# Optimization experiments

Hardware: AMD Instinct MI355X
Metric: run time of the kernel (lower is better)

The kernel has to match this reference:

```python
import jax, jax.numpy as jnp
import numpy as np

NUM_USERS = 100000
NUM_ITEMS = 10000
USER_DIM = 32
ITEM_DIM = 32
H1 = 128
H2 = 128
BATCH = 4096


def setup_inputs() -> dict:
    key = jax.random.key(0)
    ks = jax.random.split(key, 10)
    interactions = jax.random.randint(ks[0], (BATCH, 2), 0, NUM_ITEMS, dtype=jnp.int64)
    users_emb_w = jax.random.normal(ks[1], (NUM_USERS, USER_DIM), dtype=jnp.float32)
    items_emb_w = jax.random.normal(ks[2], (NUM_ITEMS, ITEM_DIM), dtype=jnp.float32)
    d_in = USER_DIM + ITEM_DIM
    w1 = jax.random.normal(ks[3], (H1, d_in), dtype=jnp.float32) / np.sqrt(d_in)
    b1 = jnp.zeros((H1,), dtype=jnp.float32)
    w2 = jax.random.normal(ks[4], (H2, H1), dtype=jnp.float32) / np.sqrt(H1)
    b2 = jnp.zeros((H2,), dtype=jnp.float32)
    head_in = NUM_ITEMS + H2
    w_head = jax.random.normal(ks[5], (NUM_ITEMS, head_in), dtype=jnp.float32) / np.sqrt(head_in)
    b_head = jnp.zeros((NUM_ITEMS,), dtype=jnp.float32)
    return {
        "interactions": interactions,
        "users_emb_w": users_emb_w,
        "items_emb_w": items_emb_w,
        "w1": w1, "b1": b1, "w2": w2, "b2": b2,
        "w_head": w_head, "b_head": b_head,
    }


def reference(interactions, users_emb_w, items_emb_w, w1, b1, w2, b2, w_head, b_head):
    users = interactions[:, 0]
    items = interactions[:, 1]
    # embedding lookups + concat -> [B, 64]
    all_embed = jnp.concatenate([users_emb_w[users], items_emb_w[items]], axis=1)
    # deep MLP (dropout p=0 -> identity)
    h = jax.nn.relu(all_embed @ w1.T + b1)
    h = jax.nn.relu(h @ w2.T + b2)
    # wide one-hot [B, num_items]
    cross = jax.nn.one_hot(items, NUM_ITEMS, dtype=h.dtype)
    head_in = jnp.concatenate([cross, h], axis=1)
    return jax.nn.sigmoid(head_in @ w_head.T + b_head)
```

## Files before the change

kernel.cpp:

```cpp
#include <hip/hip_runtime.h>


#define BATCH    4096
#define NITEMS   10000
#define HEADCOLS 10128
#define DENSEOFF 10000

typedef __attribute__((ext_vector_type(8))) short short8;
typedef __attribute__((ext_vector_type(4))) short short4v;
typedef __attribute__((ext_vector_type(4))) float floatx4;

__device__ inline unsigned short f2bf(float f) {
    unsigned u = __builtin_bit_cast(unsigned, f);
    unsigned r = (u + 0x7FFFu + ((u >> 16) & 1u)) >> 16;
    return (unsigned short)r;
}

__device__ inline float bf2f(unsigned short u) {
    unsigned x = ((unsigned)u) << 16;
    return __builtin_bit_cast(float, x);
}

__global__ __launch_bounds__(256) void k1_mlp(
    const int* __restrict__ inter,
    const float* __restrict__ U, const float* __restrict__ I,
    const float* __restrict__ w1, const float* __restrict__ b1,
    const float* __restrict__ w2, const float* __restrict__ b2,
    unsigned short* __restrict__ h2b)
{
    __shared__ float e_lds[8 * 64];
    __shared__ float h1_lds[8 * 128];
    const int t  = threadIdx.x;
    const int b0 = blockIdx.x * 8;

    for (int idx = t; idx < 8 * 64; idx += 256) {
        int b = idx >> 6, d = idx & 63;
        int u  = inter[2 * (b0 + b)];
        int it = inter[2 * (b0 + b) + 1];
        e_lds[idx] = (d < 32) ? U[(long)u * 32 + d] : I[(long)it * 32 + (d - 32)];
    }
    __syncthreads();

    const int i = t & 127;
    const int g = (t >> 7) * 4;

    {
        float acc[4];
        #pragma unroll
        for (int b = 0; b < 4; b++) acc[b] = b1[i];
        for (int d = 0; d < 64; d += 4) {
            float4 w = *(const float4*)&w1[i * 64 + d];
            #pragma unroll
            for (int b = 0; b < 4; b++) {
                float4 e = *(const float4*)&e_lds[(g + b) * 64 + d];
                acc[b] += w.x * e.x + w.y * e.y + w.z * e.z + w.w * e.w;
            }
        }
        #pragma unroll
        for (int b = 0; b < 4; b++) h1_lds[(g + b) * 128 + i] = fmaxf(acc[b], 0.f);
    }
    __syncthreads();

    {
        float acc[4];
        #pragma unroll
        for (int b = 0; b < 4; b++) acc[b] = b2[i];
        for (int k = 0; k < 128; k += 4) {
            float4 w = *(const float4*)&w2[i * 128 + k];
            #pragma unroll
            for (int b = 0; b < 4; b++) {
                float4 h = *(const float4*)&h1_lds[(g + b) * 128 + k];
                acc[b] += w.x * h.x + w.y * h.y + w.z * h.z + w.w * h.w;
            }
        }
        #pragma unroll
        for (int b = 0; b < 4; b++)
            h2b[(long)(b0 + g + b) * 128 + i] = f2bf(fmaxf(acc[b], 0.f));
    }
}

#define KG_ROWS 4
__global__ __launch_bounds__(256) void kg_gather(
    const int* __restrict__ inter,
    const float* __restrict__ w_head,
    unsigned short* __restrict__ wg,
    unsigned short* __restrict__ wd)
{
    __shared__ float row_lds[HEADCOLS];
    const int t  = threadIdx.x;
    const int j0 = blockIdx.x * KG_ROWS;

    int c0[8], c1[8];
    #pragma unroll
    for (int i = 0; i < 8; i++) {
        int p = t + 256 * i;
        c0[i] = inter[4 * p + 1];
        c1[i] = inter[4 * p + 3];
    }

    for (int r = 0; r < KG_ROWS; r++) {
        const float* row = w_head + (long)(j0 + r) * HEADCOLS;
        for (int idx = t; idx < HEADCOLS / 4; idx += 256) {
            floatx4 v = __builtin_nontemporal_load((const floatx4*)row + idx);
            *(floatx4*)&row_lds[idx * 4] = v;
        }
        __syncthreads();

        unsigned* wr = (unsigned*)(wg + (long)(j0 + r) * BATCH);
        #pragma unroll
        for (int i = 0; i < 8; i++) {
            unsigned lo = f2bf(row_lds[c0[i]]);
            unsigned hi = f2bf(row_lds[c1[i]]);
            __builtin_nontemporal_store(lo | (hi << 16), &wr[t + 256 * i]);
        }
        if (t < 128) wd[(long)(j0 + r) * 128 + t] = f2bf(row_lds[DENSEOFF + t]);
        __syncthreads();
    }
}

#define LDSTR 136

__global__ __launch_bounds__(256) void k2_head(
    const unsigned short* __restrict__ h2b,
    const unsigned short* __restrict__ wd, const float* __restrict__ b_head,
    const unsigned short* __restrict__ wg, float* __restrict__ out)
{
    __shared__ short A_lds[128 * LDSTR];
    __shared__ short B_lds[128 * LDSTR];

    const int t     = threadIdx.x;
    const int bbase = blockIdx.x * 128;
    const int jbase = blockIdx.y * 128;

    for (int idx = t; idx < 128 * 16; idx += 256) {
        int r = idx >> 4, s = idx & 15;
        short8 v = *(const short8*)&h2b[(long)(bbase + r) * 128 + s * 8];
        *(short8*)&A_lds[r * LDSTR + s * 8] = v;
    }
    for (int idx = t; idx < 128 * 16; idx += 256) {
        int r = idx >> 4, s = idx & 15;
        int j = jbase + r;
        short8 v;
        if (j < NITEMS) v = *(const short8*)&wd[(long)j * 128 + s * 8];
        else { v[0]=0;v[1]=0;v[2]=0;v[3]=0;v[4]=0;v[5]=0;v[6]=0;v[7]=0; }
        *(short8*)&B_lds[r * LDSTR + s * 8] = v;
    }
    __syncthreads();

    const int lane = t & 63, wave = t >> 6;
    const int wb = (wave & 1) * 64, wj = (wave >> 1) * 64;
    const int col = lane & 15, quad = lane >> 4;

    floatx4 acc[4][4];
    #pragma unroll
    for (int bi = 0; bi < 4; bi++)
        #pragma unroll
        for (int ji = 0; ji < 4; ji++)
            #pragma unroll
            for (int r = 0; r < 4; r++) acc[bi][ji][r] = 0.f;

    #pragma unroll
    for (int ks = 0; ks < 4; ks++) {
        short8 a[4], b[4];
        #pragma unroll
        for (int bi = 0; bi < 4; bi++)
            a[bi] = *(const short8*)&A_lds[(wb + bi * 16 + col) * LDSTR + ks * 32 + quad * 8];
        #pragma unroll
        for (int ji = 0; ji < 4; ji++)
            b[ji] = *(const short8*)&B_lds[(wj + ji * 16 + col) * LDSTR + ks * 32 + quad * 8];
        #pragma unroll
        for (int bi = 0; bi < 4; bi++)
            #pragma unroll
            for (int ji = 0; ji < 4; ji++)
                acc[bi][ji] = __builtin_amdgcn_mfma_f32_16x16x32_bf16(a[bi], b[ji], acc[bi][ji], 0, 0, 0);
    }

    #pragma unroll
    for (int ji = 0; ji < 4; ji++) {
        int j = jbase + wj + ji * 16 + col;
        bool jv = (j < NITEMS);
        float bias = jv ? b_head[j] : 0.f;
        const unsigned short* wgr = wg + (long)(jv ? j : 0) * BATCH + bbase;
        #pragma unroll
        for (int bi = 0; bi < 4; bi++) {
            short4v wv = *(const short4v*)&wgr[wb + bi * 16 + quad * 4];
            #pragma unroll
            for (int r = 0; r < 4; r++) {
                int bl = wb + bi * 16 + quad * 4 + r;
                float wide = bf2f((unsigned short)wv[r]);
                float x = acc[bi][ji][r] + bias + wide;
                float y = 1.f / (1.f + __expf(-x));
                if (jv) __builtin_nontemporal_store(y, &out[(long)(bbase + bl) * NITEMS + j]);
            }
        }
    }
}

__global__ __launch_bounds__(256) void k2_head_fb(
    const unsigned short* __restrict__ h2b,
    const float* __restrict__ w_head, const float* __restrict__ b_head,
    const int* __restrict__ inter, float* __restrict__ out)
{
    __shared__ short A_lds[128 * LDSTR];
    __shared__ short B_lds[128 * LDSTR];
    __shared__ int items[128];

    const int t     = threadIdx.x;
    const int bbase = blockIdx.x * 128;
    const int jbase = blockIdx.y * 128;

    if (t < 128) items[t] = inter[2 * (bbase + t) + 1];

    for (int idx = t; idx < 128 * 16; idx += 256) {
        int r = idx >> 4, s = idx & 15;
        short8 v = *(const short8*)&h2b[(long)(bbase + r) * 128 + s * 8];
        *(short8*)&A_lds[r * LDSTR + s * 8] = v;
    }
    for (int idx = t; idx < 128 * 32; idx += 256) {
        int r = idx >> 5, s = idx & 31;
        int j = jbase + r;
        short4v o4;
        if (j < NITEMS) {
            float4 w = *(const float4*)&w_head[(long)j * HEADCOLS + DENSEOFF + s * 4];
            o4[0] = (short)f2bf(w.x); o4[1] = (short)f2bf(w.y);
            o4[2] = (short)f2bf(w.z); o4[3] = (short)f2bf(w.w);
        } else {
            o4[0] = 0; o4[1] = 0; o4[2] = 0; o4[3] = 0;
        }
        *(short4v*)&B_lds[r * LDSTR + s * 4] = o4;
    }
    __syncthreads();

    const int lane = t & 63, wave = t >> 6;
    const int wb = (wave & 1) * 64, wj = (wave >> 1) * 64;
    const int col = lane & 15, quad = lane >> 4;

    floatx4 acc[4][4];
    #pragma unroll
    for (int bi = 0; bi < 4; bi++)
        #pragma unroll
        for (int ji = 0; ji < 4; ji++)
            #pragma unroll
            for (int r = 0; r < 4; r++) acc[bi][ji][r] = 0.f;

    #pragma unroll
    for (int ks = 0; ks < 4; ks++) {
        short8 a[4], b[4];
        #pragma unroll
        for (int bi = 0; bi < 4; bi++)
            a[bi] = *(const short8*)&A_lds[(wb + bi * 16 + col) * LDSTR + ks * 32 + quad * 8];
        #pragma unroll
        for (int ji = 0; ji < 4; ji++)
            b[ji] = *(const short8*)&B_lds[(wj + ji * 16 + col) * LDSTR + ks * 32 + quad * 8];
        #pragma unroll
        for (int bi = 0; bi < 4; bi++)
            #pragma unroll
            for (int ji = 0; ji < 4; ji++)
                acc[bi][ji] = __builtin_amdgcn_mfma_f32_16x16x32_bf16(a[bi], b[ji], acc[bi][ji], 0, 0, 0);
    }

    #pragma unroll
    for (int ji = 0; ji < 4; ji++) {
        int j = jbase + wj + ji * 16 + col;
        bool jv = (j < NITEMS);
        float bias = jv ? b_head[j] : 0.f;
        const float* wrow = w_head + (long)(jv ? j : 0) * HEADCOLS;
        #pragma unroll
        for (int bi = 0; bi < 4; bi++) {
            #pragma unroll
            for (int r = 0; r < 4; r++) {
                int bl = wb + bi * 16 + quad * 4 + r;
                float wide = jv ? wrow[items[bl]] : 0.f;
                float x = acc[bi][ji][r] + bias + wide;
                float y = 1.f / (1.f + __expf(-x));
                if (jv) out[(long)(bbase + bl) * NITEMS + j] = y;
            }
        }
    }
}

extern "C" void kernel_launch(void* const* d_in, const int* in_sizes, int n_in,
                              void* d_out, int out_size, void* d_ws, size_t ws_size,
                              hipStream_t stream) {
    const int*   inter = (const int*)d_in[0];
    const float* U     = (const float*)d_in[1];
    const float* I     = (const float*)d_in[2];
    const float* w1    = (const float*)d_in[3];
    const float* b1    = (const float*)d_in[4];
    const float* w2    = (const float*)d_in[5];
    const float* b2    = (const float*)d_in[6];
    const float* wh    = (const float*)d_in[7];
    const float* bh    = (const float*)d_in[8];
    float* out = (float*)d_out;

    unsigned short* h2b = (unsigned short*)d_ws;
    const size_t WG_OFF  = 1u << 20;
    const size_t WG_SIZE = (size_t)NITEMS * BATCH * 2;
    const size_t WD_OFF  = WG_OFF + WG_SIZE;
    const size_t WD_SIZE = (size_t)NITEMS * 128 * 2;

    k1_mlp<<<512, 256, 0, stream>>>(inter, U, I, w1, b1, w2, b2, h2b);

    if (ws_size >= WD_OFF + WD_SIZE) {
        unsigned short* wg = (unsigned short*)((char*)d_ws + WG_OFF);
        unsigned short* wd = (unsigned short*)((char*)d_ws + WD_OFF);
        kg_gather<<<NITEMS / KG_ROWS, 256, 0, stream>>>(inter, wh, wg, wd);
        k2_head<<<dim3(32, 79), 256, 0, stream>>>(h2b, wd, bh, wg, out);
    } else {
        k2_head_fb<<<dim3(32, 79), 256, 0, stream>>>(h2b, wh, bh, inter, out);
    }
}
```

Measured before the change: 691.3 us.

## Fuse MLP and head-weight gather into one launch with register prefetch

```diff
diff --git a/kernel.cpp b/kernel.cpp
--- a/kernel.cpp
+++ b/kernel.cpp
@@ -5,6 +5,10 @@
 #define NITEMS   10000
 #define HEADCOLS 10128
 #define DENSEOFF 10000
+#define KG_ROWS  4
+#define KG_BLOCKS (NITEMS / KG_ROWS)
+#define MLP_BLOCKS 512
+#define ROWCHUNKS 10
 
 typedef __attribute__((ext_vector_type(8))) short short8;
 typedef __attribute__((ext_vector_type(4))) short short4v;
@@ -19,6 +23,120 @@
 __device__ inline float bf2f(unsigned short u) {
     unsigned x = ((unsigned)u) << 16;
     return __builtin_bit_cast(float, x);
+}
+
+__global__ __launch_bounds__(256) void k1g(
+    const int* __restrict__ inter,
+    const float* __restrict__ U, const float* __restrict__ I,
+    const float* __restrict__ w1, const float* __restrict__ b1,
+    const float* __restrict__ w2, const float* __restrict__ b2,
+    const float* __restrict__ w_head,
+    unsigned short* __restrict__ h2b,
+    unsigned short* __restrict__ wg,
+    unsigned short* __restrict__ wd)
+{
+    __shared__ float lds[HEADCOLS];
+    const int t   = threadIdx.x;
+    const int bid = blockIdx.x;
+
+    if (bid < KG_BLOCKS) {
+        const int j0 = bid * KG_ROWS;
+
+        int c0[8], c1[8];
+        #pragma unroll
+        for (int i = 0; i < 8; i++) {
+            int p = t + 256 * i;
+            c0[i] = inter[4 * p + 1];
+            c1[i] = inter[4 * p + 3];
+        }
+
+        floatx4 buf[ROWCHUNKS];
+        {
+            const floatx4* src = (const floatx4*)(w_head + (long)j0 * HEADCOLS);
+            #pragma unroll
+            for (int i = 0; i < ROWCHUNKS; i++) {
+                int idx = t + 256 * i;
+                if (idx < HEADCOLS / 4) buf[i] = __builtin_nontemporal_load(src + idx);
+            }
+        }
+
+        for (int r = 0; r < KG_ROWS; r++) {
+            __syncthreads();
+            #pragma unroll
+            for (int i = 0; i < ROWCHUNKS; i++) {
+                int idx = t + 256 * i;
+                if (idx < HEADCOLS / 4) *(floatx4*)&lds[idx * 4] = buf[i];
+            }
+            __syncthreads();
+
+            if (r + 1 < KG_ROWS) {
+                const floatx4* src = (const floatx4*)(w_head + (long)(j0 + r + 1) * HEADCOLS);
+                #pragma unroll
+                for (int i = 0; i < ROWCHUNKS; i++) {
+                    int idx = t + 256 * i;
+                    if (idx < HEADCOLS / 4) buf[i] = __builtin_nontemporal_load(src + idx);
+                }
+            }
+
+            unsigned* wr = (unsigned*)(wg + (long)(j0 + r) * BATCH);
+            #pragma unroll
+            for (int i = 0; i < 8; i++) {
+                unsigned lo = f2bf(lds[c0[i]]);
+                unsigned hi = f2bf(lds[c1[i]]);
+                wr[t + 256 * i] = lo | (hi << 16);
+            }
+            if (t < 128) wd[(long)(j0 + r) * 128 + t] = f2bf(lds[DENSEOFF + t]);
+        }
+    } else {
+        float* e_lds  = lds;
+        float* h1_lds = lds + 512;
+        const int b0 = (bid - KG_BLOCKS) * 8;
+
+        for (int idx = t; idx < 8 * 64; idx += 256) {
+            int b = idx >> 6, d = idx & 63;
+            int u  = inter[2 * (b0 + b)];
+            int it = inter[2 * (b0 + b) + 1];
+            e_lds[idx] = (d < 32) ? U[(long)u * 32 + d] : I[(long)it * 32 + (d - 32)];
+        }
+        __syncthreads();
+
+        const int i = t & 127;
+        const int g = (t >> 7) * 4;
+
+        {
+            float acc[4];
+            #pragma unroll
+            for (int b = 0; b < 4; b++) acc[b] = b1[i];
+            for (int d = 0; d < 64; d += 4) {
+                float4 w = *(const float4*)&w1[i * 64 + d];
+                #pragma unroll
+                for (int b = 0; b < 4; b++) {
+                    float4 e = *(const float4*)&e_lds[(g + b) * 64 + d];
+                    acc[b] += w.x * e.x + w.y * e.y + w.z * e.z + w.w * e.w;
+                }
+            }
+            #pragma unroll
+            for (int b = 0; b < 4; b++) h1_lds[(g + b) * 128 + i] = fmaxf(acc[b], 0.f);
+        }
+        __syncthreads();
+
+        {
+            float acc[4];
+            #pragma unroll
+            for (int b = 0; b < 4; b++) acc[b] = b2[i];
+            for (int k = 0; k < 128; k += 4) {
+                float4 w = *(const float4*)&w2[i * 128 + k];
+                #pragma unroll
+                for (int b = 0; b < 4; b++) {
+                    float4 h = *(const float4*)&h1_lds[(g + b) * 128 + k];
+                    acc[b] += w.x * h.x + w.y * h.y + w.z * h.z + w.w * h.w;
+                }
+            }
+            #pragma unroll
+            for (int b = 0; b < 4; b++)
+                h2b[(long)(b0 + g + b) * 128 + i] = f2bf(fmaxf(acc[b], 0.f));
+        }
+    }
 }
 
 __global__ __launch_bounds__(256) void k1_mlp(
@@ -76,45 +194,6 @@
         #pragma unroll
         for (int b = 0; b < 4; b++)
             h2b[(long)(b0 + g + b) * 128 + i] = f2bf(fmaxf(acc[b], 0.f));
-    }
-}
-
-#define KG_ROWS 4
-__global__ __launch_bounds__(256) void kg_gather(
-    const int* __restrict__ inter,
-    const float* __restrict__ w_head,
-    unsigned short* __restrict__ wg,
-    unsigned short* __restrict__ wd)
-{
-    __shared__ float row_lds[HEADCOLS];
-    const int t  = threadIdx.x;
-    const int j0 = blockIdx.x * KG_ROWS;
-
-    int c0[8], c1[8];
-    #pragma unroll
-    for (int i = 0; i < 8; i++) {
-        int p = t + 256 * i;
-        c0[i] = inter[4 * p + 1];
-        c1[i] = inter[4 * p + 3];
-    }
-
-    for (int r = 0; r < KG_ROWS; r++) {
-        const float* row = w_head + (long)(j0 + r) * HEADCOLS;
-        for (int idx = t; idx < HEADCOLS / 4; idx += 256) {
-            floatx4 v = __builtin_nontemporal_load((const floatx4*)row + idx);
-            *(floatx4*)&row_lds[idx * 4] = v;
-        }
-        __syncthreads();
-
-        unsigned* wr = (unsigned*)(wg + (long)(j0 + r) * BATCH);
-        #pragma unroll
-        for (int i = 0; i < 8; i++) {
-            unsigned lo = f2bf(row_lds[c0[i]]);
-            unsigned hi = f2bf(row_lds[c1[i]]);
-            __builtin_nontemporal_store(lo | (hi << 16), &wr[t + 256 * i]);
-        }
-        if (t < 128) wd[(long)(j0 + r) * 128 + t] = f2bf(row_lds[DENSEOFF + t]);
-        __syncthreads();
     }
 }
 
@@ -299,14 +378,13 @@
     const size_t WD_OFF  = WG_OFF + WG_SIZE;
     const size_t WD_SIZE = (size_t)NITEMS * 128 * 2;
 
-    k1_mlp<<<512, 256, 0, stream>>>(inter, U, I, w1, b1, w2, b2, h2b);
-
     if (ws_size >= WD_OFF + WD_SIZE) {
         unsigned short* wg = (unsigned short*)((char*)d_ws + WG_OFF);
         unsigned short* wd = (unsigned short*)((char*)d_ws + WD_OFF);
-        kg_gather<<<NITEMS / KG_ROWS, 256, 0, stream>>>(inter, wh, wg, wd);
+        k1g<<<KG_BLOCKS + MLP_BLOCKS, 256, 0, stream>>>(inter, U, I, w1, b1, w2, b2, wh, h2b, wg, wd);
         k2_head<<<dim3(32, 79), 256, 0, stream>>>(h2b, wd, bh, wg, out);
     } else {
+        k1_mlp<<<512, 256, 0, stream>>>(inter, U, I, w1, b1, w2, b2, h2b);
         k2_head_fb<<<dim3(32, 79), 256, 0, stream>>>(h2b, wh, bh, inter, out);
     }
 }
```

New measurement: 647.0 us. -6.4%, faster.
